# Performance work log

Measured on AMD Instinct MI355X. Metric: run time of the kernel, lower is better.

## Reference

```python
import jax, jax.numpy as jnp
import numpy as np

NBINS = 256
NCH = 3


def _channel_hists(img):
    """img: [B, 3, H, W] float with values in [0, 256).
    Returns [3, 256] histogram counts, summed over the batch (matches
    cv2.calcHist per channel accumulated over images)."""
    idx = jnp.clip(img, 0.0, 255.0).astype(jnp.int32)          # bin = floor(v)
    offs = (jnp.arange(NCH, dtype=jnp.int32) * NBINS)[None, :, None, None]
    flat = (idx + offs).reshape(-1)                             # [B*3*H*W]
    h = jnp.zeros(NCH * NBINS, dtype=img.dtype).at[flat].add(1.0)
    return h.reshape(NCH, NBINS)


def _bhattacharyya_sum(h1, h2):
    """OpenCV HISTCMP_BHATTACHARYYA per channel, summed over channels.
    d = sqrt(1 - sum(sqrt(H1*H2)) / (N * sqrt(mean(H1)*mean(H2))))"""
    s = jnp.sum(jnp.sqrt(h1 * h2), axis=-1)                     # [3]
    denom = jnp.sqrt(h1.mean(-1) * h2.mean(-1)) * NBINS         # [3]
    d = jnp.sqrt(jnp.maximum(1.0 - s / denom, 0.0))
    return jnp.sum(d)


def setup_inputs() -> dict:
    key = jax.random.key(0)
    k1, k2 = jax.random.split(key)
    shape = (32, 3, 512, 512)
    # pixel values in [0, 256) like real image data
    inp = jax.random.uniform(k1, shape, dtype=jnp.float32) * 256.0
    lab = jax.random.uniform(k2, shape, dtype=jnp.float32) * 256.0
    return {"input": inp, "label": lab}


def reference(input, label):
    h_in = _channel_hists(input)    # [3, 256]
    h_lb = _channel_hists(label)    # [3, 256]
    return _bhattacharyya_sum(h_in, h_lb)
```

## Files before the change

### kernel.cpp

```cpp
#include <hip/hip_runtime.h>

#define NBINS 256
#define NCH 3
#define NHIST (2 * NCH * NBINS)
#define HW4 65536
#define BATCH 32
#define BLOCKS_PER_JOB 256
#define THREADS 256


__device__ __forceinline__ void batch4(unsigned int* lbase, float4 v) {
    const int b0 = (int)fminf(fmaxf(v.x, 0.f), 255.f);
    const int b1 = (int)fminf(fmaxf(v.y, 0.f), 255.f);
    const int b2 = (int)fminf(fmaxf(v.z, 0.f), 255.f);
    const int b3 = (int)fminf(fmaxf(v.w, 0.f), 255.f);
    const int w0 = b0 >> 2, w1 = b1 >> 2, w2 = b2 >> 2, w3 = b3 >> 2;
    unsigned int i0 = 1u << ((b0 & 3) << 3);
    unsigned int i1 = 1u << ((b1 & 3) << 3);
    unsigned int i2 = 1u << ((b2 & 3) << 3);
    unsigned int i3 = 1u << ((b3 & 3) << 3);
    unsigned int* const p0 = lbase + w0 * 64;
    unsigned int* const p1 = lbase + w1 * 64;
    unsigned int* const p2 = lbase + w2 * 64;
    unsigned int* const p3 = lbase + w3 * 64;
    const unsigned int r0 = *p0;
    const unsigned int r1 = *p1;
    const unsigned int r2 = *p2;
    const unsigned int r3 = *p3;
    if (w0 == w1) { i1 += i0; i0 = 0; }
    if (w0 == w2) { i2 += i0; i0 = 0; }
    if (w0 == w3) { i3 += i0; i0 = 0; }
    if (w1 == w2) { i2 += i1; i1 = 0; }
    if (w1 == w3) { i3 += i1; i1 = 0; }
    if (w2 == w3) { i3 += i2; i2 = 0; }
    *p0 = r0 + i0;
    *p1 = r1 + i1;
    *p2 = r2 + i2;
    *p3 = r3 + i3;
}

__global__ __launch_bounds__(THREADS) void hist_kernel(
    const float* __restrict__ a, const float* __restrict__ b,
    unsigned int* __restrict__ gh) {
    __shared__ unsigned int sh[16384];
    const int tid  = threadIdx.x;
    const int wave = tid >> 6;
    const int lane = tid & 63;

    uint4* shv = (uint4*)sh;
    #pragma unroll
    for (int i = 0; i < 16; ++i)
        shv[tid + i * THREADS] = make_uint4(0u, 0u, 0u, 0u);
    __syncthreads();

    const int job        = blockIdx.x >> 8;
    const int blockInJob = blockIdx.x & 255;
    const int arr = job / NCH;
    const int ch  = job % NCH;

    const float4* __restrict__ src = (const float4*)(arr ? b : a);
    unsigned int* const lbase = &sh[wave * 4096 + lane];
    const unsigned pos = ((unsigned)blockInJob << 8) | (unsigned)tid;

    for (int it = 0; it < BATCH / 4; ++it) {
        const int bt = it << 2;
        const float4 v0 = src[(unsigned)(((bt + 0) * NCH + ch) << 16) | pos];
        const float4 v1 = src[(unsigned)(((bt + 1) * NCH + ch) << 16) | pos];
        const float4 v2 = src[(unsigned)(((bt + 2) * NCH + ch) << 16) | pos];
        const float4 v3 = src[(unsigned)(((bt + 3) * NCH + ch) << 16) | pos];
        batch4(lbase, v0);
        batch4(lbase, v1);
        batch4(lbase, v2);
        batch4(lbase, v3);
    }
    __syncthreads();

    unsigned int sum = 0;
    const int grp = tid >> 2;
    const int sh8 = (tid & 3) << 3;
    #pragma unroll
    for (int w = 0; w < 4; ++w) {
        const unsigned int* base = &sh[w * 4096 + grp * 64];
        #pragma unroll
        for (int c = 0; c < 16; ++c) {
            const int cc = (c + tid) & 15;
            const uint4 q = *(const uint4*)(base + cc * 4);
            sum += ((q.x >> sh8) & 0xFFu) + ((q.y >> sh8) & 0xFFu)
                 + ((q.z >> sh8) & 0xFFu) + ((q.w >> sh8) & 0xFFu);
        }
    }
    atomicAdd(&gh[(arr * NCH + ch) * NBINS + tid], sum);
}

__device__ __forceinline__ double block_reduce256(double v, double* sh4) {
    const int t = threadIdx.x;
    const int lane = t & 63, w = t >> 6;
    #pragma unroll
    for (int o = 32; o > 0; o >>= 1) v += __shfl_down(v, o, 64);
    if (lane == 0) sh4[w] = v;
    __syncthreads();
    double r = sh4[0] + sh4[1] + sh4[2] + sh4[3];
    __syncthreads();
    return r;
}

__global__ __launch_bounds__(256) void bhat_kernel(
    const unsigned int* __restrict__ gh, float* __restrict__ out) {
    __shared__ double sh4[4];
    const int t = threadIdx.x;
    double result = 0.0;
    #pragma unroll
    for (int ch = 0; ch < NCH; ++ch) {
        const double h1 = (double)gh[ch * NBINS + t];
        const double h2 = (double)gh[(NCH + ch) * NBINS + t];
        const double s  = block_reduce256(sqrt(h1 * h2), sh4);
        const double s1 = block_reduce256(h1, sh4);
        const double s2 = block_reduce256(h2, sh4);
        const double denom = sqrt((s1 / (double)NBINS) * (s2 / (double)NBINS)) * (double)NBINS;
        const double v = 1.0 - s / denom;
        result += sqrt(v > 0.0 ? v : 0.0);
    }
    if (t == 0) out[0] = (float)result;
}

extern "C" void kernel_launch(void* const* d_in, const int* in_sizes, int n_in,
                              void* d_out, int out_size, void* d_ws, size_t ws_size,
                              hipStream_t stream) {
    const float* input = (const float*)d_in[0];
    const float* label = (const float*)d_in[1];
    float* out = (float*)d_out;
    unsigned int* gh = (unsigned int*)d_ws;

    hipMemsetAsync(gh, 0, NHIST * sizeof(unsigned int), stream);

    hist_kernel<<<6 * BLOCKS_PER_JOB, THREADS, 0, stream>>>(input, label, gh);
    bhat_kernel<<<1, 256, 0, stream>>>(gh, out);
}
```

Before: 219.4 us.

## Prefetch next batch in registers and interleave two per-wave sub-histograms

Each block now has 128 threads, and the grid doubles to keep full coverage. Each wave owns two private byte-packed LDS sub-histograms, alternated so the read of one quad overlaps the write of the other. The next 8 float4 loads are prefetched into registers while the current 8 are being binned, to hide global latency behind the LDS read-modify-write chain. The final reduction has each thread merge two bins. The 64 KB LDS footprint per block now serves only 2 waves, so resident waves per CU drop, and more register pressure comes from the prefetch buffers.

```diff
diff --git a/kernel.cpp b/kernel.cpp
--- a/kernel.cpp
+++ b/kernel.cpp
@@ -3,40 +3,49 @@
 #define NBINS 256
 #define NCH 3
 #define NHIST (2 * NCH * NBINS)
-#define HW4 65536
 #define BATCH 32
-#define BLOCKS_PER_JOB 256
-#define THREADS 256
+#define THREADS 128
+#define BLOCKS_PER_JOB 512
 
 
-__device__ __forceinline__ void batch4(unsigned int* lbase, float4 v) {
+struct Quad {
+    unsigned int* p0; unsigned int* p1; unsigned int* p2; unsigned int* p3;
+    unsigned int r0, r1, r2, r3;
+    unsigned int i0, i1, i2, i3;
+    int w0, w1, w2, w3;
+};
+
+__device__ __forceinline__ void quad_read(unsigned int* lbase, float4 v, Quad& q) {
     const int b0 = (int)fminf(fmaxf(v.x, 0.f), 255.f);
     const int b1 = (int)fminf(fmaxf(v.y, 0.f), 255.f);
     const int b2 = (int)fminf(fmaxf(v.z, 0.f), 255.f);
     const int b3 = (int)fminf(fmaxf(v.w, 0.f), 255.f);
-    const int w0 = b0 >> 2, w1 = b1 >> 2, w2 = b2 >> 2, w3 = b3 >> 2;
-    unsigned int i0 = 1u << ((b0 & 3) << 3);
-    unsigned int i1 = 1u << ((b1 & 3) << 3);
-    unsigned int i2 = 1u << ((b2 & 3) << 3);
-    unsigned int i3 = 1u << ((b3 & 3) << 3);
-    unsigned int* const p0 = lbase + w0 * 64;
-    unsigned int* const p1 = lbase + w1 * 64;
-    unsigned int* const p2 = lbase + w2 * 64;
-    unsigned int* const p3 = lbase + w3 * 64;
-    const unsigned int r0 = *p0;
-    const unsigned int r1 = *p1;
-    const unsigned int r2 = *p2;
-    const unsigned int r3 = *p3;
-    if (w0 == w1) { i1 += i0; i0 = 0; }
-    if (w0 == w2) { i2 += i0; i0 = 0; }
-    if (w0 == w3) { i3 += i0; i0 = 0; }
-    if (w1 == w2) { i2 += i1; i1 = 0; }
-    if (w1 == w3) { i3 += i1; i1 = 0; }
-    if (w2 == w3) { i3 += i2; i2 = 0; }
-    *p0 = r0 + i0;
-    *p1 = r1 + i1;
-    *p2 = r2 + i2;
-    *p3 = r3 + i3;
+    q.w0 = b0 >> 2; q.w1 = b1 >> 2; q.w2 = b2 >> 2; q.w3 = b3 >> 2;
+    q.i0 = 1u << ((b0 & 3) << 3);
+    q.i1 = 1u << ((b1 & 3) << 3);
+    q.i2 = 1u << ((b2 & 3) << 3);
+    q.i3 = 1u << ((b3 & 3) << 3);
+    q.p0 = lbase + q.w0 * 64;
+    q.p1 = lbase + q.w1 * 64;
+    q.p2 = lbase + q.w2 * 64;
+    q.p3 = lbase + q.w3 * 64;
+    q.r0 = *q.p0;
+    q.r1 = *q.p1;
+    q.r2 = *q.p2;
+    q.r3 = *q.p3;
+}
+
+__device__ __forceinline__ void quad_write(Quad& q) {
+    if (q.w0 == q.w1) { q.i1 += q.i0; q.i0 = 0; }
+    if (q.w0 == q.w2) { q.i2 += q.i0; q.i0 = 0; }
+    if (q.w0 == q.w3) { q.i3 += q.i0; q.i0 = 0; }
+    if (q.w1 == q.w2) { q.i2 += q.i1; q.i1 = 0; }
+    if (q.w1 == q.w3) { q.i3 += q.i1; q.i1 = 0; }
+    if (q.w2 == q.w3) { q.i3 += q.i2; q.i2 = 0; }
+    *q.p0 = q.r0 + q.i0;
+    *q.p1 = q.r1 + q.i1;
+    *q.p2 = q.r2 + q.i2;
+    *q.p3 = q.r3 + q.i3;
 }
 
 __global__ __launch_bounds__(THREADS) void hist_kernel(
@@ -49,47 +58,74 @@
 
     uint4* shv = (uint4*)sh;
     #pragma unroll
-    for (int i = 0; i < 16; ++i)
+    for (int i = 0; i < 32; ++i)
         shv[tid + i * THREADS] = make_uint4(0u, 0u, 0u, 0u);
     __syncthreads();
 
-    const int job        = blockIdx.x >> 8;
-    const int blockInJob = blockIdx.x & 255;
+    const int job        = blockIdx.x >> 9;
+    const int blockInJob = blockIdx.x & 511;
     const int arr = job / NCH;
     const int ch  = job % NCH;
 
     const float4* __restrict__ src = (const float4*)(arr ? b : a);
-    unsigned int* const lbase = &sh[wave * 4096 + lane];
-    const unsigned pos = ((unsigned)blockInJob << 8) | (unsigned)tid;
+    unsigned int* const baseA = &sh[wave * 8192 + lane];
+    unsigned int* const baseB = baseA + 4096;
+    const unsigned pos = ((unsigned)blockInJob << 7) | (unsigned)tid;
 
-    for (int it = 0; it < BATCH / 4; ++it) {
-        const int bt = it << 2;
-        const float4 v0 = src[(unsigned)(((bt + 0) * NCH + ch) << 16) | pos];
-        const float4 v1 = src[(unsigned)(((bt + 1) * NCH + ch) << 16) | pos];
-        const float4 v2 = src[(unsigned)(((bt + 2) * NCH + ch) << 16) | pos];
-        const float4 v3 = src[(unsigned)(((bt + 3) * NCH + ch) << 16) | pos];
-        batch4(lbase, v0);
-        batch4(lbase, v1);
-        batch4(lbase, v2);
-        batch4(lbase, v3);
+#define LOADIDX(bt) ((unsigned)((((bt) * NCH + ch) << 16) | pos))
+
+    float4 c0 = src[LOADIDX(0)], c1 = src[LOADIDX(1)];
+    float4 c2 = src[LOADIDX(2)], c3 = src[LOADIDX(3)];
+    float4 c4 = src[LOADIDX(4)], c5 = src[LOADIDX(5)];
+    float4 c6 = src[LOADIDX(6)], c7 = src[LOADIDX(7)];
+
+    #pragma unroll
+    for (int it = 0; it < BATCH / 8; ++it) {
+        float4 n0, n1, n2, n3, n4, n5, n6, n7;
+        if (it < 3) {
+            const int nbt = (it + 1) << 3;
+            n0 = src[LOADIDX(nbt + 0)]; n1 = src[LOADIDX(nbt + 1)];
+            n2 = src[LOADIDX(nbt + 2)]; n3 = src[LOADIDX(nbt + 3)];
+            n4 = src[LOADIDX(nbt + 4)]; n5 = src[LOADIDX(nbt + 5)];
+            n6 = src[LOADIDX(nbt + 6)]; n7 = src[LOADIDX(nbt + 7)];
+        }
+        Quad qa, qb;
+        quad_read(baseA, c0, qa);
+        quad_read(baseB, c1, qb);
+        quad_write(qa); quad_read(baseA, c2, qa);
+        quad_write(qb); quad_read(baseB, c3, qb);
+        quad_write(qa); quad_read(baseA, c4, qa);
+        quad_write(qb); quad_read(baseB, c5, qb);
+        quad_write(qa); quad_read(baseA, c6, qa);
+        quad_write(qb); quad_read(baseB, c7, qb);
+        quad_write(qa);
+        quad_write(qb);
+        if (it < 3) {
+            c0 = n0; c1 = n1; c2 = n2; c3 = n3;
+            c4 = n4; c5 = n5; c6 = n6; c7 = n7;
+        }
     }
     __syncthreads();
 
-    unsigned int sum = 0;
-    const int grp = tid >> 2;
-    const int sh8 = (tid & 3) << 3;
     #pragma unroll
-    for (int w = 0; w < 4; ++w) {
-        const unsigned int* base = &sh[w * 4096 + grp * 64];
+    for (int h = 0; h < 2; ++h) {
+        const int bin = tid + (h << 7);
+        const int grp = bin >> 2;
+        const int sh8 = (bin & 3) << 3;
+        unsigned int s = 0;
         #pragma unroll
-        for (int c = 0; c < 16; ++c) {
-            const int cc = (c + tid) & 15;
-            const uint4 q = *(const uint4*)(base + cc * 4);
-            sum += ((q.x >> sh8) & 0xFFu) + ((q.y >> sh8) & 0xFFu)
-                 + ((q.z >> sh8) & 0xFFu) + ((q.w >> sh8) & 0xFFu);
+        for (int wr = 0; wr < 4; ++wr) {
+            const unsigned int* base = &sh[wr * 4096 + grp * 64];
+            #pragma unroll
+            for (int c = 0; c < 16; ++c) {
+                const int cc = (c + tid) & 15;
+                const uint4 q = *(const uint4*)(base + cc * 4);
+                s += ((q.x >> sh8) & 0xFFu) + ((q.y >> sh8) & 0xFFu)
+                   + ((q.z >> sh8) & 0xFFu) + ((q.w >> sh8) & 0xFFu);
+            }
         }
+        atomicAdd(&gh[(arr * NCH + ch) * NBINS + bin], s);
     }
-    atomicAdd(&gh[(arr * NCH + ch) * NBINS + tid], sum);
 }
 
 __device__ __forceinline__ double block_reduce256(double v, double* sh4) {
```

Result: slower. 230.2 us (+4.9%).
